# Kernel tuning notes

Hardware: AMD Instinct MI355X
Metric: run time of the kernel (lower is better)

## Reference

```python
import jax, jax.numpy as jnp
import numpy as np

N, E, IN, HID, H, G, OUT = 50000, 800000, 128, 96, 8, 64, 10
D = HID // H  # per-head dim = 12


def setup_inputs() -> dict:
    key = jax.random.key(0)
    ks = jax.random.split(key, 24)
    s = 0.1
    inp = {
        'x': jax.random.normal(ks[0], (N, IN), jnp.float32),
        'src': jax.random.randint(ks[1], (E,), 0, N, jnp.int32),
        'dst': jax.random.randint(ks[2], (E,), 0, N, jnp.int32),
        'graph_id': jax.random.randint(ks[3], (N,), 0, G, jnp.int32),
        # GraphConv layers (norm='both', weight + bias)
        'W1': jax.random.normal(ks[4], (IN, HID), jnp.float32) * s,
        'b1': jnp.zeros((HID,), jnp.float32),
        'W2': jax.random.normal(ks[5], (HID, HID), jnp.float32) * s,
        'b2': jnp.zeros((HID,), jnp.float32),
        # 3 GATv2 layers, stacked params
        'Ws': jax.random.normal(ks[6], (3, HID, HID), jnp.float32) * s,
        'bs': jnp.zeros((3, HID), jnp.float32),
        'Wd': jax.random.normal(ks[7], (3, HID, HID), jnp.float32) * s,
        'bd': jnp.zeros((3, HID), jnp.float32),
        'attn': jax.random.normal(ks[8], (3, H, D), jnp.float32) * s,
        # classifier MLP (dropout is identity at inference)
        'Wc1': jax.random.normal(ks[9], (HID, HID), jnp.float32) * s,
        'bc1': jnp.zeros((HID,), jnp.float32),
        'Wc2': jax.random.normal(ks[10], (HID, HID // 2), jnp.float32) * s,
        'bc2': jnp.zeros((HID // 2,), jnp.float32),
        'Wc3': jax.random.normal(ks[11], (HID // 2, OUT), jnp.float32) * s,
        'bc3': jnp.zeros((OUT,), jnp.float32),
    }
    return inp


def _graph_conv(h, W, b, src, dst):
    # DGL GraphConv, norm='both', allow_zero_in_degree (degrees clamped to >=1)
    ones = jnp.ones((E,), h.dtype)
    deg_out = jnp.clip(jax.ops.segment_sum(ones, src, N), 1.0)
    deg_in = jnp.clip(jax.ops.segment_sum(ones, dst, N), 1.0)
    h = (h * (deg_out ** -0.5)[:, None]) @ W          # [N, out]
    agg = jax.ops.segment_sum(h[src], dst, N)          # sum over in-edges
    return agg * (deg_in ** -0.5)[:, None] + b


def _gatv2(h, Ws, bs, Wd, bd, attn, src, dst):
    fs = (h @ Ws + bs).reshape(N, H, D)
    fd = (h @ Wd + bd).reshape(N, H, D)
    e = jax.nn.leaky_relu(fs[src] + fd[dst], 0.2)      # [E, H, D]
    logits = jnp.einsum('ehd,hd->eh', e, attn)         # [E, H]
    # edge softmax over incoming edges of each dst node
    m = jax.ops.segment_max(logits, dst, N)            # [N, H]
    ex = jnp.exp(logits - m[dst])
    den = jax.ops.segment_sum(ex, dst, N)              # [N, H]
    a = ex / den[dst]                                  # [E, H]
    rst = jax.ops.segment_sum(a[:, :, None] * fs[src], dst, N)  # [N, H, D]
    return jax.nn.relu(rst).reshape(N, HID)            # activation=relu, then view


def reference(x, src, dst, graph_id, W1, b1, W2, b2, Ws, bs, Wd, bd, attn,
              Wc1, bc1, Wc2, bc2, Wc3, bc3):
    h = jax.nn.relu(_graph_conv(x, W1, b1, src, dst))
    h = jax.nn.relu(_graph_conv(h, W2, b2, src, dst))
    for i in range(3):
        h = _gatv2(h, Ws[i], bs[i], Wd[i], bd[i], attn[i], src, dst)
    # dgl.max_nodes: per-graph max readout
    hg = jax.ops.segment_max(h, graph_id, G)           # [G, HID]
    z = jax.nn.relu(hg @ Wc1 + bc1)
    z = jax.nn.relu(z @ Wc2 + bc2)
    return z @ Wc3 + bc3                               # [G, OUT]
```

## Files before the change

kernel.cpp:

```cpp
#include <hip/hip_runtime.h>
#include <hip/hip_bf16.h>

#define Nn 50000
#define Ee 800000
#define INF_ 128
#define HIDF 96
#define HH 8
#define DD 12
#define GG 64
#define OUTF 10

#define SCAN_CHUNK 512
#define SCAN_BLOCKS ((Nn + SCAN_CHUNK - 1) / SCAN_CHUNK)
#define NSB ((Nn + 255) / 256)
#define RB 128

#define HCHK 256
#define HCHKE (Ee / HCHK)
#define NW 12512
#define DBIN 64

__global__ __launch_bounds__(512) void hist_lds(const int* __restrict__ src,
                                                const int* __restrict__ dst,
                                                unsigned int* __restrict__ partS,
                                                unsigned int* __restrict__ partD,
                                                unsigned char* __restrict__ edge_slot) {
    __shared__ unsigned int hS[NW];
    __shared__ unsigned int hD[NW];
    int b = blockIdx.x, t = threadIdx.x;
    for (int i = t; i < NW; i += 512) { hS[i] = 0u; hD[i] = 0u; }
    __syncthreads();
    int base = b * HCHKE;
    for (int i = t; i < HCHKE; i += 512) {
        int d = dst[base + i];
        unsigned int old = atomicAdd(&hD[d >> 2], 1u << ((d & 3) * 8));
        edge_slot[base + i] = (unsigned char)((old >> ((d & 3) * 8)) & 0xFFu);
        int s = src[base + i];
        atomicAdd(&hS[s >> 2], 1u << ((s & 3) * 8));
    }
    __syncthreads();
    for (int i = t; i < NW; i += 512) {
        partD[(size_t)b * NW + i] = hD[i];
        partS[(size_t)b * NW + i] = hS[i];
    }
}

__global__ __launch_bounds__(256) void hist_scan(unsigned int* __restrict__ partD,
                                                 const unsigned int* __restrict__ partS,
                                                 int* __restrict__ cnt_in,
                                                 float* __restrict__ degI_is,
                                                 float* __restrict__ degO_is,
                                                 int* __restrict__ dcnt) {
    __shared__ int hbin[DBIN];
    int t = threadIdx.x;
    if (t < DBIN) hbin[t] = 0;
    __syncthreads();
    int w = blockIdx.x * 256 + t;
    if (w < NW) {
        unsigned int run = 0u, totS = 0u;
        for (int b = 0; b < HCHK; ++b) {
            size_t idx = (size_t)b * NW + w;
            unsigned int v = partD[idx];
            partD[idx] = run;
            run += v;
            totS += partS[idx];
        }
#pragma unroll
        for (int j = 0; j < 4; ++j) {
            int k = w * 4 + j;
            if (k < Nn) {
                int di = (int)((run >> (j * 8)) & 0xFFu);
                int dо = (int)((totS >> (j * 8)) & 0xFFu);
                cnt_in[k] = di;
                degI_is[k] = rsqrtf((float)max(di, 1));
                degO_is[k] = rsqrtf((float)max(dо, 1));
                atomicAdd(&hbin[DBIN - 1 - min(di, DBIN - 1)], 1);
            }
        }
    }
    __syncthreads();
    if (t < DBIN && hbin[t]) atomicAdd(&dcnt[t], hbin[t]);
}

__global__ __launch_bounds__(256) void scan1_kernel(const int* __restrict__ cnt,
                                                    int* __restrict__ row_start,
                                                    int* __restrict__ blk_sum, int N) {
    __shared__ int part[256];
    int t = threadIdx.x;
    int base = blockIdx.x * SCAN_CHUNK;
    int i0 = base + 2 * t, i1 = i0 + 1;
    int a = (i0 < N) ? cnt[i0] : 0;
    int b = (i1 < N) ? cnt[i1] : 0;
    int s = a + b;
    part[t] = s;
    __syncthreads();
    for (int off = 1; off < 256; off <<= 1) {
        int v = (t >= off) ? part[t - off] : 0;
        __syncthreads();
        part[t] += v;
        __syncthreads();
    }
    int excl = part[t] - s;
    if (i0 < N) row_start[i0] = excl;
    if (i1 < N) row_start[i1] = excl + a;
    if (t == 255) blk_sum[blockIdx.x] = part[255];
}

__global__ __launch_bounds__(128) void scan2_kernel(const int* __restrict__ blk_sum,
                                                    int* __restrict__ blk_off,
                                                    int* __restrict__ row_start,
                                                    const int* __restrict__ dcnt,
                                                    int* __restrict__ dcur, int N) {
    __shared__ int part[128];
    int t = threadIdx.x;
    if (blockIdx.x == 0) {
        int v0 = (t < SCAN_BLOCKS) ? blk_sum[t] : 0;
        part[t] = v0;
        __syncthreads();
        for (int off = 1; off < 128; off <<= 1) {
            int v = (t >= off) ? part[t - off] : 0;
            __syncthreads();
            part[t] += v;
            __syncthreads();
        }
        blk_off[t] = part[t] - v0;
        if (t == 127) row_start[N] = part[127];
    } else {
        int v0 = (t < DBIN) ? dcnt[t] : 0;
        part[t] = v0;
        __syncthreads();
        for (int off = 1; off < DBIN; off <<= 1) {
            int v = (t >= off) ? part[t - off] : 0;
            __syncthreads();
            part[t] += v;
            __syncthreads();
        }
        if (t < DBIN) dcur[t] = part[t] - v0;
    }
}

__global__ __launch_bounds__(256) void scan3_kernel(int* __restrict__ row_start,
                                                    const int* __restrict__ blk_off,
                                                    const int* __restrict__ cnt_in,
                                                    int* __restrict__ dcur,
                                                    int* __restrict__ perm, int N) {
    int t = threadIdx.x;
    if (blockIdx.x < SCAN_BLOCKS) {
        int base = blockIdx.x * SCAN_CHUNK;
        int off = blk_off[blockIdx.x];
        int i0 = base + 2 * t, i1 = i0 + 1;
        if (i0 < N) row_start[i0] += off;
        if (i1 < N) row_start[i1] += off;
    } else {
        __shared__ int lh[DBIN];
        __shared__ int lbase[DBIN];
        if (t < DBIN) lh[t] = 0;
        __syncthreads();
        int n = (blockIdx.x - SCAN_BLOCKS) * 256 + t;
        int bin = 0, lslot = 0;
        if (n < N) {
            bin = DBIN - 1 - min(cnt_in[n], DBIN - 1);
            lslot = atomicAdd(&lh[bin], 1);
        }
        __syncthreads();
        if (t < DBIN) lbase[t] = lh[t] ? atomicAdd(&dcur[t], lh[t]) : 0;
        __syncthreads();
        if (n < N) perm[lbase[bin] + lslot] = n;
    }
}

__global__ __launch_bounds__(512) void fill_kernel(const int* __restrict__ src,
                                                   const int* __restrict__ dst,
                                                   const int* __restrict__ row_start,
                                                   const unsigned int* __restrict__ partD,
                                                   const unsigned char* __restrict__ edge_slot,
                                                   int* __restrict__ csr_src) {
    int b = blockIdx.x, t = threadIdx.x;
    int base = b * HCHKE;
    size_t po = (size_t)b * NW;
    for (int i = t; i < HCHKE; i += 512) {
        int e = base + i;
        int d = dst[e];
        int cb = (int)((partD[po + (d >> 2)] >> ((d & 3) * 8)) & 0xFFu);
        csr_src[row_start[d] + cb + (int)edge_slot[e]] = src[e];
    }
}

__global__ __launch_bounds__(192) void gemm96(const float* __restrict__ A, int K,
                                              const float* __restrict__ W,
                                              const float* __restrict__ bias,
                                              const float* __restrict__ rowScale,
                                              float* __restrict__ out, int N) {
    __shared__ float A_lds[64 * 36];
    __shared__ float W_lds[32 * 96];
    const int t = threadIdx.x;
    const int row0 = blockIdx.x * 64;
    const int tcol = t % 24;
    const int trow = t / 24;
    float acc[8][4];
#pragma unroll
    for (int i = 0; i < 8; ++i)
#pragma unroll
        for (int j = 0; j < 4; ++j) acc[i][j] = 0.f;

    for (int k0 = 0; k0 < K; k0 += 32) {
        for (int i = t; i < 32 * 24; i += 192) {
            ((float4*)W_lds)[i] = ((const float4*)W)[(size_t)k0 * 24 + i];
        }
        for (int i = t; i < 64 * 8; i += 192) {
            int r = i / 8, kk = i % 8;
            int gr = row0 + r;
            float4 v = make_float4(0.f, 0.f, 0.f, 0.f);
            if (gr < N) {
                v = *((const float4*)(A + (size_t)gr * K + k0 + kk * 4));
                if (rowScale) {
                    float s = rowScale[gr];
                    v.x *= s; v.y *= s; v.z *= s; v.w *= s;
                }
            }
            *((float4*)(A_lds + r * 36 + kk * 4)) = v;
        }
        __syncthreads();
#pragma unroll
        for (int kk4 = 0; kk4 < 8; ++kk4) {
            float4 a[8];
#pragma unroll
            for (int i = 0; i < 8; ++i)
                a[i] = *((const float4*)(A_lds + (trow + 8 * i) * 36 + kk4 * 4));
#pragma unroll
            for (int kk = 0; kk < 4; ++kk) {
                float4 wv = *((const float4*)(W_lds + (kk4 * 4 + kk) * 96 + tcol * 4));
#pragma unroll
                for (int i = 0; i < 8; ++i) {
                    float av = (kk == 0) ? a[i].x : (kk == 1) ? a[i].y : (kk == 2) ? a[i].z : a[i].w;
                    acc[i][0] = fmaf(av, wv.x, acc[i][0]);
                    acc[i][1] = fmaf(av, wv.y, acc[i][1]);
                    acc[i][2] = fmaf(av, wv.z, acc[i][2]);
                    acc[i][3] = fmaf(av, wv.w, acc[i][3]);
                }
            }
        }
        __syncthreads();
    }
    float4 b4 = bias ? *((const float4*)(bias + tcol * 4)) : make_float4(0.f, 0.f, 0.f, 0.f);
#pragma unroll
    for (int i = 0; i < 8; ++i) {
        int gr = row0 + trow + 8 * i;
        if (gr < N) {
            float4 o = make_float4(acc[i][0] + b4.x, acc[i][1] + b4.y,
                                   acc[i][2] + b4.z, acc[i][3] + b4.w);
            *((float4*)(out + (size_t)gr * 96 + tcol * 4)) = o;
        }
    }
}

__global__ __launch_bounds__(192) void gemm96x2(const float* __restrict__ A,
                                                const float* __restrict__ W1_, const float* __restrict__ b1_,
                                                const float* __restrict__ W2_, const float* __restrict__ b2_,
                                                float* __restrict__ out1, float* __restrict__ out2, int N) {
    __shared__ float A_lds[64 * 36];
    __shared__ float W_lds[2 * 32 * 96];
    const int t = threadIdx.x;
    const int row0 = blockIdx.x * 64;
    const int tcol = t % 24;
    const int trow = t / 24;
    float acc1[8][4], acc2[8][4];
#pragma unroll
    for (int i = 0; i < 8; ++i)
#pragma unroll
        for (int j = 0; j < 4; ++j) { acc1[i][j] = 0.f; acc2[i][j] = 0.f; }

    for (int k0 = 0; k0 < 96; k0 += 32) {
        for (int i = t; i < 32 * 24; i += 192) {
            ((float4*)W_lds)[i] = ((const float4*)W1_)[(size_t)k0 * 24 + i];
            ((float4*)(W_lds + 32 * 96))[i] = ((const float4*)W2_)[(size_t)k0 * 24 + i];
        }
        for (int i = t; i < 64 * 8; i += 192) {
            int r = i / 8, kk = i % 8;
            int gr = row0 + r;
            float4 v = make_float4(0.f, 0.f, 0.f, 0.f);
            if (gr < N) v = *((const float4*)(A + (size_t)gr * 96 + k0 + kk * 4));
            *((float4*)(A_lds + r * 36 + kk * 4)) = v;
        }
        __syncthreads();
#pragma unroll
        for (int kk4 = 0; kk4 < 8; ++kk4) {
            float4 a[8];
#pragma unroll
            for (int i = 0; i < 8; ++i)
                a[i] = *((const float4*)(A_lds + (trow + 8 * i) * 36 + kk4 * 4));
#pragma unroll
            for (int kk = 0; kk < 4; ++kk) {
                float4 wv1 = *((const float4*)(W_lds + (kk4 * 4 + kk) * 96 + tcol * 4));
                float4 wv2 = *((const float4*)(W_lds + 32 * 96 + (kk4 * 4 + kk) * 96 + tcol * 4));
#pragma unroll
                for (int i = 0; i < 8; ++i) {
                    float av = (kk == 0) ? a[i].x : (kk == 1) ? a[i].y : (kk == 2) ? a[i].z : a[i].w;
                    acc1[i][0] = fmaf(av, wv1.x, acc1[i][0]);
                    acc1[i][1] = fmaf(av, wv1.y, acc1[i][1]);
                    acc1[i][2] = fmaf(av, wv1.z, acc1[i][2]);
                    acc1[i][3] = fmaf(av, wv1.w, acc1[i][3]);
                    acc2[i][0] = fmaf(av, wv2.x, acc2[i][0]);
                    acc2[i][1] = fmaf(av, wv2.y, acc2[i][1]);
                    acc2[i][2] = fmaf(av, wv2.z, acc2[i][2]);
                    acc2[i][3] = fmaf(av, wv2.w, acc2[i][3]);
                }
            }
        }
        __syncthreads();
    }
    float4 bb1 = *((const float4*)(b1_ + tcol * 4));
    float4 bb2 = *((const float4*)(b2_ + tcol * 4));
#pragma unroll
    for (int i = 0; i < 8; ++i) {
        int gr = row0 + trow + 8 * i;
        if (gr < N) {
            float4 o1 = make_float4(acc1[i][0] + bb1.x, acc1[i][1] + bb1.y,
                                    acc1[i][2] + bb1.z, acc1[i][3] + bb1.w);
            float4 o2 = make_float4(acc2[i][0] + bb2.x, acc2[i][1] + bb2.y,
                                    acc2[i][2] + bb2.z, acc2[i][3] + bb2.w);
            *((float4*)(out1 + (size_t)gr * 96 + tcol * 4)) = o1;
            *((float4*)(out2 + (size_t)gr * 96 + tcol * 4)) = o2;
        }
    }
}

__global__ __launch_bounds__(192) void gc_agg(const float* __restrict__ hW,
                                              const int* __restrict__ row_start,
                                              const int* __restrict__ csr_src,
                                              const float* __restrict__ degI_is,
                                              const float* __restrict__ bias,
                                              const int* __restrict__ perm,
                                              float* __restrict__ hout, int N) {
    int tid = blockIdx.x * 192 + threadIdx.x;
    int p = tid / 24;
    int c = (tid % 24) * 4;
    if (p >= N) return;
    int n = perm[p];
    int beg = row_start[n], end = row_start[n + 1];
    float4 s = make_float4(0.f, 0.f, 0.f, 0.f);
    int e = beg;
    for (; e + 4 <= end; e += 4) {
        int i0 = csr_src[e], i1 = csr_src[e + 1], i2 = csr_src[e + 2], i3 = csr_src[e + 3];
        float4 v0 = *(const float4*)(hW + (size_t)i0 * 96 + c);
        float4 v1 = *(const float4*)(hW + (size_t)i1 * 96 + c);
        float4 v2 = *(const float4*)(hW + (size_t)i2 * 96 + c);
        float4 v3 = *(const float4*)(hW + (size_t)i3 * 96 + c);
        s.x += (v0.x + v1.x) + (v2.x + v3.x);
        s.y += (v0.y + v1.y) + (v2.y + v3.y);
        s.z += (v0.z + v1.z) + (v2.z + v3.z);
        s.w += (v0.w + v1.w) + (v2.w + v3.w);
    }
    for (; e < end; ++e) {
        int i0 = csr_src[e];
        float4 v0 = *(const float4*)(hW + (size_t)i0 * 96 + c);
        s.x += v0.x; s.y += v0.y; s.z += v0.z; s.w += v0.w;
    }
    float dn = degI_is[n];
    float4 b = *(const float4*)(bias + c);
    float4 o;
    o.x = fmaxf(fmaf(s.x, dn, b.x), 0.f);
    o.y = fmaxf(fmaf(s.y, dn, b.y), 0.f);
    o.z = fmaxf(fmaf(s.z, dn, b.z), 0.f);
    o.w = fmaxf(fmaf(s.w, dn, b.w), 0.f);
    *(float4*)(hout + (size_t)n * 96 + c) = o;
}

__global__ __launch_bounds__(256) void gat_agg(const float* __restrict__ fs,
                                               const float* __restrict__ fd,
                                               const float* __restrict__ attn,
                                               const int* __restrict__ row_start,
                                               const int* __restrict__ csr_src,
                                               const int* __restrict__ perm,
                                               float* __restrict__ hout, int N) {
    int tid = blockIdx.x * 256 + threadIdx.x;
    int p = tid >> 3, hd = tid & 7;
    if (p >= N) return;
    int n = perm[p];
    float att[12], fdv[12];
    {
        const float4* ap = (const float4*)(attn + hd * 12);
        float4 a0 = ap[0], a1 = ap[1], a2 = ap[2];
        att[0]=a0.x; att[1]=a0.y; att[2]=a0.z; att[3]=a0.w;
        att[4]=a1.x; att[5]=a1.y; att[6]=a1.z; att[7]=a1.w;
        att[8]=a2.x; att[9]=a2.y; att[10]=a2.z; att[11]=a2.w;
        const float4* dp = (const float4*)(fd + (size_t)n * 96 + hd * 12);
        float4 d0 = dp[0], d1 = dp[1], d2 = dp[2];
        fdv[0]=d0.x; fdv[1]=d0.y; fdv[2]=d0.z; fdv[3]=d0.w;
        fdv[4]=d1.x; fdv[5]=d1.y; fdv[6]=d1.z; fdv[7]=d1.w;
        fdv[8]=d2.x; fdv[9]=d2.y; fdv[10]=d2.z; fdv[11]=d2.w;
    }
    int beg = row_start[n], end = row_start[n + 1];
    float m0 = -3.0e38f, den0 = 0.f, m1 = -3.0e38f, den1 = 0.f;
    float A0[12], A1[12];
#pragma unroll
    for (int d = 0; d < 12; ++d) { A0[d] = 0.f; A1[d] = 0.f; }

    auto proc = [&](const float4& s0, const float4& s1, const float4& s2,
                    float& m, float& den, float* acc) {
        float fsv[12];
        fsv[0]=s0.x; fsv[1]=s0.y; fsv[2]=s0.z; fsv[3]=s0.w;
        fsv[4]=s1.x; fsv[5]=s1.y; fsv[6]=s1.z; fsv[7]=s1.w;
        fsv[8]=s2.x; fsv[9]=s2.y; fsv[10]=s2.z; fsv[11]=s2.w;
        float logit = 0.f;
#pragma unroll
        for (int d = 0; d < 12; ++d) {
            float u = fsv[d] + fdv[d];
            u = u > 0.f ? u : 0.2f * u;
            logit = fmaf(u, att[d], logit);
        }
        float nm = fmaxf(m, logit);
        float cc = __expf(m - nm);
        float w  = __expf(logit - nm);
        den = fmaf(den, cc, w);
#pragma unroll
        for (int d = 0; d < 12; ++d) acc[d] = fmaf(acc[d], cc, w * fsv[d]);
        m = nm;
    };

    int e = beg;
    for (; e + 4 <= end; e += 4) {
        int i0 = csr_src[e], i1 = csr_src[e + 1], i2 = csr_src[e + 2], i3 = csr_src[e + 3];
        const float4* p0 = (const float4*)(fs + (size_t)i0 * 96 + hd * 12);
        const float4* p1 = (const float4*)(fs + (size_t)i1 * 96 + hd * 12);
        const float4* p2 = (const float4*)(fs + (size_t)i2 * 96 + hd * 12);
        const float4* p3 = (const float4*)(fs + (size_t)i3 * 96 + hd * 12);
        float4 a0 = p0[0], a1 = p0[1], a2 = p0[2];
        float4 b0 = p1[0], b1 = p1[1], b2 = p1[2];
        float4 c0 = p2[0], c1 = p2[1], c2 = p2[2];
        float4 d0 = p3[0], d1 = p3[1], d2 = p3[2];
        proc(a0, a1, a2, m0, den0, A0);
        proc(b0, b1, b2, m1, den1, A1);
        proc(c0, c1, c2, m0, den0, A0);
        proc(d0, d1, d2, m1, den1, A1);
    }
    for (; e < end; ++e) {
        int i0 = csr_src[e];
        const float4* p0 = (const float4*)(fs + (size_t)i0 * 96 + hd * 12);
        float4 a0 = p0[0], a1 = p0[1], a2 = p0[2];
        proc(a0, a1, a2, m0, den0, A0);
    }
    float nm = fmaxf(m0, m1);
    float c0 = __expf(m0 - nm), c1 = __expf(m1 - nm);
    float den = den0 * c0 + den1 * c1;
    float inv = den > 0.f ? 1.f / den : 0.f;
    float* op = hout + (size_t)n * 96 + hd * 12;
#pragma unroll
    for (int d = 0; d < 12; ++d)
        op[d] = fmaxf((A0[d] * c0 + A1[d] * c1) * inv, 0.f);
}

__global__ __launch_bounds__(384) void readout_partial(const float* __restrict__ h,
                                                       const int* __restrict__ graph_id,
                                                       float* __restrict__ partial, int N) {
    __shared__ int lhg[GG * 96];
    int t = threadIdx.x;
    for (int i = t; i < GG * 96; i += 384) lhg[i] = 0;
    __syncthreads();
    int f = t % 96, nl = t / 96;
    for (int n0 = blockIdx.x * 4; n0 < N; n0 += RB * 4) {
        int n = n0 + nl;
        if (n < N) {
            int g = graph_id[n];
            float v = h[(size_t)n * 96 + f];
            atomicMax(&lhg[g * 96 + f], __float_as_int(v));
        }
    }
    __syncthreads();
    for (int i = t; i < GG * 96; i += 384)
        partial[(size_t)blockIdx.x * (GG * 96) + i] = __int_as_float(lhg[i]);
}

__global__ void readout_reduce(const float* __restrict__ partial, float* __restrict__ hg) {
    int i = blockIdx.x * 256 + threadIdx.x;
    if (i < GG * 96) {
        float m = 0.f;
        for (int b = 0; b < RB; ++b) m = fmaxf(m, partial[(size_t)b * (GG * 96) + i]);
        hg[i] = m;
    }
}

__global__ __launch_bounds__(96) void mlp_kernel(const float* __restrict__ hg,
                                                 const float* __restrict__ Wc1, const float* __restrict__ bc1,
                                                 const float* __restrict__ Wc2, const float* __restrict__ bc2,
                                                 const float* __restrict__ Wc3, const float* __restrict__ bc3,
                                                 float* __restrict__ out) {
    int g = blockIdx.x;
    int t = threadIdx.x;
    __shared__ float z0[96], z1[96], z2[48];
    z0[t] = hg[(size_t)g * 96 + t];
    __syncthreads();
    float s = bc1[t];
    for (int k = 0; k < 96; ++k) s = fmaf(z0[k], Wc1[k * 96 + t], s);
    z1[t] = fmaxf(s, 0.f);
    __syncthreads();
    if (t < 48) {
        float s2 = bc2[t];
        for (int k = 0; k < 96; ++k) s2 = fmaf(z1[k], Wc2[k * 48 + t], s2);
        z2[t] = fmaxf(s2, 0.f);
    }
    __syncthreads();
    if (t < 10) {
        float s3 = bc3[t];
        for (int k = 0; k < 48; ++k) s3 = fmaf(z2[k], Wc3[k * 10 + t], s3);
        out[(size_t)g * 10 + t] = s3;
    }
}

extern "C" void kernel_launch(void* const* d_in, const int* in_sizes, int n_in,
                              void* d_out, int out_size, void* d_ws, size_t ws_size,
                              hipStream_t stream) {
    const float* x        = (const float*)d_in[0];
    const int*   src      = (const int*)d_in[1];
    const int*   dst      = (const int*)d_in[2];
    const int*   graph_id = (const int*)d_in[3];
    const float* W1  = (const float*)d_in[4];
    const float* b1  = (const float*)d_in[5];
    const float* W2  = (const float*)d_in[6];
    const float* b2  = (const float*)d_in[7];
    const float* Ws  = (const float*)d_in[8];
    const float* bs  = (const float*)d_in[9];
    const float* Wd  = (const float*)d_in[10];
    const float* bd  = (const float*)d_in[11];
    const float* attn = (const float*)d_in[12];
    const float* Wc1 = (const float*)d_in[13];
    const float* bc1 = (const float*)d_in[14];
    const float* Wc2 = (const float*)d_in[15];
    const float* bc2 = (const float*)d_in[16];
    const float* Wc3 = (const float*)d_in[17];
    const float* bc3 = (const float*)d_in[18];
    float* out = (float*)d_out;

    char* ws = (char*)d_ws;
    size_t off = 0;
    auto alloc = [&](size_t bytes) {
        char* p = ws + off;
        off = (off + bytes + 255) & ~(size_t)255;
        return p;
    };
    int*   cnt_in    = (int*)alloc(Nn * 4);
    int*   row_start = (int*)alloc((Nn + 1) * 4);
    unsigned char* edge_slot = (unsigned char*)alloc(Ee);
    int*   csr_src   = (int*)alloc(Ee * 4);
    int*   perm      = (int*)alloc(Nn * 4);
    float* degI_is   = (float*)alloc(Nn * 4);
    float* degO_is   = (float*)alloc(Nn * 4);
    float* bufH      = (float*)alloc((size_t)Nn * 96 * 4);
    float* bufT      = (float*)alloc((size_t)Nn * 96 * 4);
    float* bufFd     = (float*)alloc((size_t)Nn * 96 * 4);
    float* hg        = (float*)alloc(GG * 96 * 4);
    float* partial   = (float*)alloc((size_t)RB * GG * 96 * 4);
    int*   blk_sum   = (int*)alloc(128 * 4);
    int*   blk_off   = (int*)alloc(128 * 4);
    int*   dcnt      = (int*)alloc(DBIN * 4);
    int*   dcur      = (int*)alloc(DBIN * 4);

    unsigned int* partS = (unsigned int*)bufT;
    unsigned int* partD = (unsigned int*)bufFd;

    hipMemsetAsync(dcnt, 0, DBIN * 4, stream);

    hist_lds<<<HCHK, 512, 0, stream>>>(src, dst, partS, partD, edge_slot);
    hist_scan<<<(NW + 255) / 256, 256, 0, stream>>>(partD, partS, cnt_in, degI_is, degO_is, dcnt);
    scan1_kernel<<<SCAN_BLOCKS, 256, 0, stream>>>(cnt_in, row_start, blk_sum, Nn);
    scan2_kernel<<<2, 128, 0, stream>>>(blk_sum, blk_off, row_start, dcnt, dcur, Nn);
    scan3_kernel<<<SCAN_BLOCKS + NSB, 256, 0, stream>>>(row_start, blk_off, cnt_in, dcur, perm, Nn);
    fill_kernel<<<HCHK, 512, 0, stream>>>(src, dst, row_start, partD, edge_slot, csr_src);

    int gemm_blocks = (Nn + 63) / 64;
    int agg_blocks  = (Nn * 24 + 191) / 192;
    int gat_blocks  = (Nn * 8 + 255) / 256;

    gemm96<<<gemm_blocks, 192, 0, stream>>>(x, 128, W1, nullptr, degO_is, bufT, Nn);
    gc_agg<<<agg_blocks, 192, 0, stream>>>(bufT, row_start, csr_src, degI_is, b1, perm, bufH, Nn);
    gemm96<<<gemm_blocks, 192, 0, stream>>>(bufH, 96, W2, nullptr, degO_is, bufT, Nn);
    gc_agg<<<agg_blocks, 192, 0, stream>>>(bufT, row_start, csr_src, degI_is, b2, perm, bufH, Nn);

    for (int l = 0; l < 3; ++l) {
        const float* Wsl = Ws + (size_t)l * 96 * 96;
        const float* bsl = bs + (size_t)l * 96;
        const float* Wdl = Wd + (size_t)l * 96 * 96;
        const float* bdl = bd + (size_t)l * 96;
        const float* atl = attn + (size_t)l * 96;
        gemm96x2<<<gemm_blocks, 192, 0, stream>>>(bufH, Wsl, bsl, Wdl, bdl, bufT, bufFd, Nn);
        gat_agg<<<gat_blocks, 256, 0, stream>>>(bufT, bufFd, atl, row_start, csr_src, perm, bufH, Nn);
    }

    readout_partial<<<RB, 384, 0, stream>>>(bufH, graph_id, partial, Nn);
    readout_reduce<<<(GG * 96 + 255) / 256, 256, 0, stream>>>(partial, hg);
    mlp_kernel<<<GG, 96, 0, stream>>>(hg, Wc1, bc1, Wc2, bc2, Wc3, bc3, out);
}
```

Measured before the change: 634.1 us.

## Stage full weights in LDS and stream A rows directly from global memory

Both dense GEMM kernels now load the entire weight matrix into LDS once per block and read activation rows straight from global memory into registers, dropping the per-K-chunk A staging and the barriers inside the loop. Out-of-range rows are clamped to the last row instead of zero-filled, and their results are still masked on store. The row scale is applied in registers. The larger LDS footprint (48-72 KB) and launch_bounds(192,1) may lower occupancy, and each thread's uncoalesced strided global reads of A rows rely on the cache to serve them.

```diff
diff --git a/kernel.cpp b/kernel.cpp
--- a/kernel.cpp
+++ b/kernel.cpp
@@ -186,61 +186,57 @@
     }
 }
 
-__global__ __launch_bounds__(192) void gemm96(const float* __restrict__ A, int K,
-                                              const float* __restrict__ W,
-                                              const float* __restrict__ bias,
-                                              const float* __restrict__ rowScale,
-                                              float* __restrict__ out, int N) {
-    __shared__ float A_lds[64 * 36];
-    __shared__ float W_lds[32 * 96];
+__global__ __launch_bounds__(192, 1) void gemm96(const float* __restrict__ A, int K,
+                                                 const float* __restrict__ W,
+                                                 const float* __restrict__ bias,
+                                                 const float* __restrict__ rowScale,
+                                                 float* __restrict__ out, int N) {
+    __shared__ float W_lds[128 * 96];
     const int t = threadIdx.x;
     const int row0 = blockIdx.x * 64;
     const int tcol = t % 24;
     const int trow = t / 24;
+
+    for (int i = t; i < K * 24; i += 192)
+        ((float4*)W_lds)[i] = ((const float4*)W)[i];
+
+    const float* Ap[8];
+    float sc[8];
+#pragma unroll
+    for (int i = 0; i < 8; ++i) {
+        int gr = row0 + trow + 8 * i;
+        gr = gr < N ? gr : N - 1;
+        Ap[i] = A + (size_t)gr * K;
+        sc[i] = rowScale ? rowScale[gr] : 1.f;
+    }
     float acc[8][4];
 #pragma unroll
     for (int i = 0; i < 8; ++i)
 #pragma unroll
         for (int j = 0; j < 4; ++j) acc[i][j] = 0.f;
 
-    for (int k0 = 0; k0 < K; k0 += 32) {
-        for (int i = t; i < 32 * 24; i += 192) {
-            ((float4*)W_lds)[i] = ((const float4*)W)[(size_t)k0 * 24 + i];
-        }
-        for (int i = t; i < 64 * 8; i += 192) {
-            int r = i / 8, kk = i % 8;
-            int gr = row0 + r;
-            float4 v = make_float4(0.f, 0.f, 0.f, 0.f);
-            if (gr < N) {
-                v = *((const float4*)(A + (size_t)gr * K + k0 + kk * 4));
-                if (rowScale) {
-                    float s = rowScale[gr];
-                    v.x *= s; v.y *= s; v.z *= s; v.w *= s;
-                }
+    __syncthreads();
+
+#pragma unroll 4
+    for (int k = 0; k < K; k += 4) {
+        float4 a[8];
+#pragma unroll
+        for (int i = 0; i < 8; ++i) {
+            a[i] = *((const float4*)(Ap[i] + k));
+            a[i].x *= sc[i]; a[i].y *= sc[i]; a[i].z *= sc[i]; a[i].w *= sc[i];
+        }
+#pragma unroll
+        for (int kk = 0; kk < 4; ++kk) {
+            float4 wv = *((const float4*)(W_lds + (k + kk) * 96 + tcol * 4));
+#pragma unroll
+            for (int i = 0; i < 8; ++i) {
+                float av = (kk == 0) ? a[i].x : (kk == 1) ? a[i].y : (kk == 2) ? a[i].z : a[i].w;
+                acc[i][0] = fmaf(av, wv.x, acc[i][0]);
+                acc[i][1] = fmaf(av, wv.y, acc[i][1]);
+                acc[i][2] = fmaf(av, wv.z, acc[i][2]);
+                acc[i][3] = fmaf(av, wv.w, acc[i][3]);
             }
-            *((float4*)(A_lds + r * 36 + kk * 4)) = v;
-        }
-        __syncthreads();
-#pragma unroll
-        for (int kk4 = 0; kk4 < 8; ++kk4) {
-            float4 a[8];
-#pragma unroll
-            for (int i = 0; i < 8; ++i)
-                a[i] = *((const float4*)(A_lds + (trow + 8 * i) * 36 + kk4 * 4));
-#pragma unroll
-            for (int kk = 0; kk < 4; ++kk) {
-                float4 wv = *((const float4*)(W_lds + (kk4 * 4 + kk) * 96 + tcol * 4));
-#pragma unroll
-                for (int i = 0; i < 8; ++i) {
-                    float av = (kk == 0) ? a[i].x : (kk == 1) ? a[i].y : (kk == 2) ? a[i].z : a[i].w;
-                    acc[i][0] = fmaf(av, wv.x, acc[i][0]);
-                    acc[i][1] = fmaf(av, wv.y, acc[i][1]);
-                    acc[i][2] = fmaf(av, wv.z, acc[i][2]);
-                    acc[i][3] = fmaf(av, wv.w, acc[i][3]);
-                }
-            }
-        }
-        __syncthreads();
+        }
     }
     float4 b4 = bias ? *((const float4*)(bias + tcol * 4)) : make_float4(0.f, 0.f, 0.f, 0.f);
 #pragma unroll
@@ -254,60 +250,59 @@
     }
 }
 
-__global__ __launch_bounds__(192) void gemm96x2(const float* __restrict__ A,
-                                                const float* __restrict__ W1_, const float* __restrict__ b1_,
-                                                const float* __restrict__ W2_, const float* __restrict__ b2_,
-                                                float* __restrict__ out1, float* __restrict__ out2, int N) {
-    __shared__ float A_lds[64 * 36];
-    __shared__ float W_lds[2 * 32 * 96];
+__global__ __launch_bounds__(192, 1) void gemm96x2(const float* __restrict__ A,
+                                                   const float* __restrict__ W1_, const float* __restrict__ b1_,
+                                                   const float* __restrict__ W2_, const float* __restrict__ b2_,
+                                                   float* __restrict__ out1, float* __restrict__ out2, int N) {
+    __shared__ float W_lds[2 * 96 * 96];
     const int t = threadIdx.x;
     const int row0 = blockIdx.x * 64;
     const int tcol = t % 24;
     const int trow = t / 24;
+
+    for (int i = t; i < 96 * 24; i += 192) {
+        ((float4*)W_lds)[i] = ((const float4*)W1_)[i];
+        ((float4*)(W_lds + 96 * 96))[i] = ((const float4*)W2_)[i];
+    }
+
+    const float* Ap[8];
+#pragma unroll
+    for (int i = 0; i < 8; ++i) {
+        int gr = row0 + trow + 8 * i;
+        gr = gr < N ? gr : N - 1;
+        Ap[i] = A + (size_t)gr * 96;
+    }
     float acc1[8][4], acc2[8][4];
 #pragma unroll
     for (int i = 0; i < 8; ++i)
 #pragma unroll
         for (int j = 0; j < 4; ++j) { acc1[i][j] = 0.f; acc2[i][j] = 0.f; }
 
-    for (int k0 = 0; k0 < 96; k0 += 32) {
-        for (int i = t; i < 32 * 24; i += 192) {
-            ((float4*)W_lds)[i] = ((const float4*)W1_)[(size_t)k0 * 24 + i];
-            ((float4*)(W_lds + 32 * 96))[i] = ((const float4*)W2_)[(size_t)k0 * 24 + i];
-        }
-        for (int i = t; i < 64 * 8; i += 192) {
-            int r = i / 8, kk = i % 8;
-            int gr = row0 + r;
-            float4 v = make_float4(0.f, 0.f, 0.f, 0.f);
-            if (gr < N) v = *((const float4*)(A + (size_t)gr * 96 + k0 + kk * 4));
-            *((float4*)(A_lds + r * 36 + kk * 4)) = v;
-        }
-        __syncthreads();
-#pragma unroll
-        for (int kk4 = 0; kk4 < 8; ++kk4) {
-            float4 a[8];
-#pragma unroll
-            for (int i = 0; i < 8; ++i)
-                a[i] = *((const float4*)(A_lds + (trow + 8 * i) * 36 + kk4 * 4));
-#pragma unroll
-            for (int kk = 0; kk < 4; ++kk) {
-                float4 wv1 = *((const float4*)(W_lds + (kk4 * 4 + kk) * 96 + tcol * 4));
-                float4 wv2 = *((const float4*)(W_lds + 32 * 96 + (kk4 * 4 + kk) * 96 + tcol * 4));
-#pragma unroll
-                for (int i = 0; i < 8; ++i) {
-                    float av = (kk == 0) ? a[i].x : (kk == 1) ? a[i].y : (kk == 2) ? a[i].z : a[i].w;
-                    acc1[i][0] = fmaf(av, wv1.x, acc1[i][0]);
-                    acc1[i][1] = fmaf(av, wv1.y, acc1[i][1]);
-                    acc1[i][2] = fmaf(av, wv1.z, acc1[i][2]);
-                    acc1[i][3] = fmaf(av, wv1.w, acc1[i][3]);
-                    acc2[i][0] = fmaf(av, wv2.x, acc2[i][0]);
-                    acc2[i][1] = fmaf(av, wv2.y, acc2[i][1]);
-                    acc2[i][2] = fmaf(av, wv2.z, acc2[i][2]);
-                    acc2[i][3] = fmaf(av, wv2.w, acc2[i][3]);
-                }
+    __syncthreads();
+
+#pragma unroll 2
+    for (int k = 0; k < 96; k += 4) {
+        float4 a[8];
+#pragma unroll
+        for (int i = 0; i < 8; ++i)
+            a[i] = *((const float4*)(Ap[i] + k));
+#pragma unroll
+        for (int kk = 0; kk < 4; ++kk) {
+            float4 wv1 = *((const float4*)(W_lds + (k + kk) * 96 + tcol * 4));
+            float4 wv2 = *((const float4*)(W_lds + 96 * 96 + (k + kk) * 96 + tcol * 4));
+#pragma unroll
+            for (int i = 0; i < 8; ++i) {
+                float av = (kk == 0) ? a[i].x : (kk == 1) ? a[i].y : (kk == 2) ? a[i].z : a[i].w;
+                acc1[i][0] = fmaf(av, wv1.x, acc1[i][0]);
+                acc1[i][1] = fmaf(av, wv1.y, acc1[i][1]);
+                acc1[i][2] = fmaf(av, wv1.z, acc1[i][2]);
+                acc1[i][3] = fmaf(av, wv1.w, acc1[i][3]);
+                acc2[i][0] = fmaf(av, wv2.x, acc2[i][0]);
+                acc2[i][1] = fmaf(av, wv2.y, acc2[i][1]);
+                acc2[i][2] = fmaf(av, wv2.z, acc2[i][2]);
+                acc2[i][3] = fmaf(av, wv2.w, acc2[i][3]);
             }
         }
-        __syncthreads();
     }
     float4 bb1 = *((const float4*)(b1_ + tcol * 4));
     float4 bb2 = *((const float4*)(b2_ + tcol * 4));
```

New measurement: 656.0 us. +3.5%, slower.
